# Optimization experiments

Hardware: AMD Instinct MI355X
Metric: run time of the kernel (lower is better)

## Reference

```python
import jax, jax.numpy as jnp
import numpy as np
import math

EMB = 2048
N_Q = 32
N_KV = 8
HEAD = EMB // N_Q  # 64
N_REP = N_Q // N_KV  # 4
B, T = 2, 2048
ROPE_BASE = 10000.0


def setup_inputs() -> dict:
    key = jax.random.key(0)
    ks = jax.random.split(key, 9)
    s = 0.02
    return {
        "x": jax.random.normal(ks[0], (B, T, EMB), jnp.float32),
        "Wq": jax.random.normal(ks[1], (EMB, EMB), jnp.float32) * s,
        "bq": jax.random.normal(ks[2], (EMB,), jnp.float32) * s,
        "Wk": jax.random.normal(ks[3], (EMB, N_KV * HEAD), jnp.float32) * s,
        "bk": jax.random.normal(ks[4], (N_KV * HEAD,), jnp.float32) * s,
        "Wv": jax.random.normal(ks[5], (EMB, N_KV * HEAD), jnp.float32) * s,
        "bv": jax.random.normal(ks[6], (N_KV * HEAD,), jnp.float32) * s,
        "Wo": jax.random.normal(ks[7], (EMB, EMB), jnp.float32) * s,
        "bo": jax.random.normal(ks[8], (EMB,), jnp.float32) * s,
    }


def _rope_cos_sin(t, dim, dtype):
    inv_freq = 1.0 / (ROPE_BASE ** (jnp.arange(0, dim, 2, dtype=jnp.float32) / dim))
    freqs = jnp.arange(t, dtype=jnp.float32)[:, None] * inv_freq[None, :]  # (T, D/2)
    emb = jnp.concatenate([freqs, freqs], axis=-1)  # (T, D)
    return jnp.cos(emb).astype(dtype), jnp.sin(emb).astype(dtype)


def _rotate_half(x):
    d = x.shape[-1] // 2
    return jnp.concatenate([-x[..., d:], x[..., :d]], axis=-1)


def reference(x, Wq, bq, Wk, bk, Wv, bv, Wo, bo):
    b, t, c = x.shape
    q = (x @ Wq + bq).reshape(b, t, N_Q, HEAD)
    k = (x @ Wk + bk).reshape(b, t, N_KV, HEAD)
    v = (x @ Wv + bv).reshape(b, t, N_KV, HEAD)

    cos, sin = _rope_cos_sin(t, HEAD, x.dtype)  # (T, HEAD)
    cos = cos[None, :, None, :]
    sin = sin[None, :, None, :]
    q = q * cos + _rotate_half(q) * sin
    k = k * cos + _rotate_half(k) * sin

    # (B, H, T, D)
    q = q.transpose(0, 2, 1, 3)
    k = k.transpose(0, 2, 1, 3)
    v = v.transpose(0, 2, 1, 3)

    # repeat_kv: expand kv heads to match query heads
    k = jnp.repeat(k, N_REP, axis=1)
    v = jnp.repeat(v, N_REP, axis=1)

    scale = 1.0 / math.sqrt(HEAD)
    att = jnp.einsum("bhqd,bhkd->bhqk", q, k) * scale
    causal = jnp.tril(jnp.ones((t, t), dtype=bool))
    att = jnp.where(causal[None, None], att, jnp.finfo(att.dtype).min)
    att = jax.nn.softmax(att, axis=-1)

    y = jnp.einsum("bhqk,bhkd->bhqd", att, v)
    y = y.transpose(0, 2, 1, 3).reshape(b, t, c)
    return y @ Wo + bo
```

## Files before the change

### kernel.cpp

```cpp
#include <hip/hip_runtime.h>
#include <hip/hip_bf16.h>
#include <cstdint>
#include <cstddef>

typedef __attribute__((ext_vector_type(4))) float f32x4;
typedef __attribute__((ext_vector_type(8))) short bf16x8;

#define B_    2
#define T_    2048
#define EMB_  2048
#define NQ_   32
#define NKV_  8
#define HEAD_ 64
#define NTOT_ 3072
#define M_    (B_ * T_)
#define QBLK_ 128
#define NK_   32

#define MFMA_ __builtin_amdgcn_mfma_f32_16x16x32_bf16

__device__ __forceinline__ unsigned short f2bf(float f) {
  union { float f; unsigned int u; } v; v.f = f;
  unsigned int r = v.u + 0x7fffu + ((v.u >> 16) & 1u);
  return (unsigned short)(r >> 16);
}

__device__ __forceinline__ float bf2f(unsigned short u) {
  union { unsigned int u; float f; } v; v.u = (unsigned int)u << 16; return v.f;
}

__device__ __forceinline__ unsigned int pk_bf16(float lo, float hi) {
  __hip_bfloat162 h = __float22bfloat162_rn(make_float2(lo, hi));
  union { __hip_bfloat162 h; unsigned int u; } c; c.h = h;
  return c.u;
}

__device__ __forceinline__ float ex2(float x) {
  float r;
  asm("v_exp_f32 %0, %1" : "=v"(r) : "v"(x));
  return r;
}

__device__ __forceinline__ void gload_lds16(const void* g, void* l) {
  __builtin_amdgcn_global_load_lds(
      (const __attribute__((address_space(1))) void*)g,
      (__attribute__((address_space(3))) void*)l, 16, 0, 0);
}


__global__ void cvt_bf16_kernel(const float* __restrict__ src,
                                unsigned short* __restrict__ dst, int n4) {
  int i = blockIdx.x * blockDim.x + threadIdx.x;
  if (i >= n4) return;
  float4 v = ((const float4*)src)[i];
  unsigned long long pk =
      (unsigned long long)f2bf(v.x) |
      ((unsigned long long)f2bf(v.y) << 16) |
      ((unsigned long long)f2bf(v.z) << 32) |
      ((unsigned long long)f2bf(v.w) << 48);
  *(unsigned long long*)(dst + (size_t)i * 4) = pk;
}

__global__ void transpose_cvt_kernel(const float* __restrict__ src,
                                     unsigned short* __restrict__ dst,
                                     int R, int C) {
  __shared__ float tile[32][33];
  int c0 = blockIdx.x * 32, r0 = blockIdx.y * 32;
  int tx = threadIdx.x, ty = threadIdx.y;
#pragma unroll
  for (int k = 0; k < 4; ++k)
    tile[ty + 8 * k][tx] = src[(size_t)(r0 + ty + 8 * k) * C + c0 + tx];
  __syncthreads();
#pragma unroll
  for (int k = 0; k < 4; ++k)
    dst[(size_t)(c0 + ty + 8 * k) * R + r0 + tx] = f2bf(tile[tx][ty + 8 * k]);
}

__global__ void concat_bias_kernel(const float* __restrict__ bq,
                                   const float* __restrict__ bk,
                                   const float* __restrict__ bv,
                                   float* __restrict__ dst) {
  int i = blockIdx.x * 256 + threadIdx.x;
  if (i < 2048) dst[i] = bq[i];
  else if (i < 2560) dst[i] = bk[i - 2048];
  else if (i < 3072) dst[i] = bv[i - 2560];
}

#define L2_10000 13.2877123795494f
#define QSCALE_  0.18033688011112043f

__global__ void rope_q_kernel(const unsigned short* __restrict__ qkv,
                              unsigned short* __restrict__ Qh) {
  int idx = blockIdx.x * 256 + threadIdx.x;
  int i  = idx & 31;
  int h  = (idx >> 5) & 31;
  int bt = idx >> 10;
  int t  = bt & (T_ - 1);
  int b  = bt >> 11;
  float invf = exp2f(-(float)i * (L2_10000 / 32.f));
  float ang = (float)t * invf;
  float s, c; sincosf(ang, &s, &c);
  const unsigned short* row = qkv + (size_t)bt * NTOT_ + h * 64;
  float x1 = bf2f(row[i]), x2 = bf2f(row[i + 32]);
  unsigned short* q = Qh + ((size_t)(b * NQ_ + h) * T_ + t) * HEAD_;
  q[i]      = f2bf((x1 * c - x2 * s) * QSCALE_);
  q[i + 32] = f2bf((x2 * c + x1 * s) * QSCALE_);
}

__global__ void rope_k_kernel(const unsigned short* __restrict__ qkv,
                              unsigned short* __restrict__ Kh) {
  int idx = blockIdx.x * 256 + threadIdx.x;
  int i  = idx & 31;
  int kh = (idx >> 5) & 7;
  int bt = idx >> 8;
  int t  = bt & (T_ - 1);
  int b  = bt >> 11;
  float invf = exp2f(-(float)i * (L2_10000 / 32.f));
  float ang = (float)t * invf;
  float s, c; sincosf(ang, &s, &c);
  const unsigned short* row = qkv + (size_t)bt * NTOT_ + 2048 + kh * 64;
  float x1 = bf2f(row[i]), x2 = bf2f(row[i + 32]);
  unsigned short* kp = Kh + ((size_t)(b * NKV_ + kh) * T_ + t) * HEAD_;
  kp[i]      = f2bf(x1 * c - x2 * s);
  kp[i + 32] = f2bf(x2 * c + x1 * s);
}

__global__ void vt_kernel(const unsigned short* __restrict__ qkv,
                          unsigned short* __restrict__ Vt) {
  int idx = blockIdx.x * 256 + threadIdx.x;
  int t  = idx & (T_ - 1);
  int d  = (idx >> 11) & 63;
  int kh = (idx >> 17) & 7;
  int b  = idx >> 20;
  Vt[((size_t)((b * NKV_ + kh) * 64 + d)) * T_ + t] =
      qkv[(size_t)(b * T_ + t) * NTOT_ + 2560 + kh * 64 + d];
}


__launch_bounds__(512, 4)
__global__ void gemm_qkv_3ph(const unsigned short* __restrict__ A,
                             const unsigned short* __restrict__ BT,
                             const float* __restrict__ bias,
                             unsigned short* __restrict__ C) {
  __shared__ unsigned short sh[2 * 20480];
  const int tid = threadIdx.x;
  const int lane = tid & 63, l16 = lane & 15, lg = lane >> 4;
  const int wave = tid >> 6, wm = wave >> 2, wn = wave & 3;
  const int bid = blockIdx.x;
  const int sw = (bid & 7) * 64 + (bid >> 3);
  const int mt = sw & 31, nt = sw >> 5;
  const int m0 = mt * 128, n0 = nt * 192;
  const int arow = tid >> 3;
  const int usrc = (tid & 7) ^ (arow & 7);
  const int swz = l16 & 7;
  const int uo0 = (lg ^ swz) << 3;
  const int uo1 = ((4 + lg) ^ swz) << 3;

  f32x4 acc[4][3];
#pragma unroll
  for (int i = 0; i < 4; ++i)
#pragma unroll
    for (int j = 0; j < 3; ++j) acc[i][j] = (f32x4){0.f, 0.f, 0.f, 0.f};

  auto STG = [&](int u) {
    if (u >= 5 * NK_) return;
    const int kt = u / 5, j = u % 5;
    char* bufb = (char*)sh + (kt & 1) * 40960;
    if (j < 2) {
      gload_lds16(A + (size_t)(m0 + j * 64 + arow) * 2048 + kt * 64 + usrc * 8,
                  bufb + j * 8192 + tid * 16);
    } else {
      const int jj = j - 2;
      gload_lds16(BT + (size_t)(n0 + jj * 64 + arow) * 2048 + kt * 64 + usrc * 8,
                  bufb + 16384 + jj * 8192 + tid * 16);
    }
  };

#pragma unroll
  for (int u = 0; u < 7; ++u) STG(u);
  asm volatile("s_waitcnt vmcnt(2)" ::: "memory");
  __builtin_amdgcn_s_barrier();

  for (int t = 0; t < NK_; ++t) {
    const unsigned short* Ab = sh + (t & 1) * 20480;
    const unsigned short* Bb = Ab + 8192;

    bf16x8 af[4][2], bfr[2];
#pragma unroll
    for (int fi = 0; fi < 4; ++fi) {
      const int ro = (fi * 32 + wm * 16 + l16) * 64;
      af[fi][0] = *(const bf16x8*)(Ab + ro + uo0);
      af[fi][1] = *(const bf16x8*)(Ab + ro + uo1);
    }
    {
      const int ro = (wn * 16 + l16) * 64;
      bfr[0] = *(const bf16x8*)(Bb + ro + uo0);
      bfr[1] = *(const bf16x8*)(Bb + ro + uo1);
    }
    STG(7 + 5 * t);  STG(8 + 5 * t);
    __builtin_amdgcn_s_barrier();
    asm volatile("s_waitcnt lgkmcnt(0)" ::: "memory");
    __builtin_amdgcn_sched_barrier(0);
    __builtin_amdgcn_s_setprio(1);
#pragma unroll
    for (int fi = 0; fi < 4; ++fi) {
      acc[fi][0] = MFMA_(af[fi][0], bfr[0], acc[fi][0], 0, 0, 0);
      acc[fi][0] = MFMA_(af[fi][1], bfr[1], acc[fi][0], 0, 0, 0);
    }
    __builtin_amdgcn_s_setprio(0);
    __builtin_amdgcn_s_barrier();

    {
      const int ro = (64 + wn * 16 + l16) * 64;
      bfr[0] = *(const bf16x8*)(Bb + ro + uo0);
      bfr[1] = *(const bf16x8*)(Bb + ro + uo1);
    }
    STG(9 + 5 * t);  STG(10 + 5 * t);
    __builtin_amdgcn_s_barrier();
    asm volatile("s_waitcnt lgkmcnt(0)" ::: "memory");
    __builtin_amdgcn_sched_barrier(0);
    __builtin_amdgcn_s_setprio(1);
#pragma unroll
    for (int fi = 0; fi < 4; ++fi) {
      acc[fi][1] = MFMA_(af[fi][0], bfr[0], acc[fi][1], 0, 0, 0);
      acc[fi][1] = MFMA_(af[fi][1], bfr[1], acc[fi][1], 0, 0, 0);
    }
    __builtin_amdgcn_s_setprio(0);
    __builtin_amdgcn_s_barrier();

    {
      const int ro = (128 + wn * 16 + l16) * 64;
      bfr[0] = *(const bf16x8*)(Bb + ro + uo0);
      bfr[1] = *(const bf16x8*)(Bb + ro + uo1);
    }
    STG(11 + 5 * t);
    __builtin_amdgcn_s_barrier();
    asm volatile("s_waitcnt lgkmcnt(0)" ::: "memory");
    __builtin_amdgcn_sched_barrier(0);
    __builtin_amdgcn_s_setprio(1);
#pragma unroll
    for (int fi = 0; fi < 4; ++fi) {
      acc[fi][2] = MFMA_(af[fi][0], bfr[0], acc[fi][2], 0, 0, 0);
      acc[fi][2] = MFMA_(af[fi][1], bfr[1], acc[fi][2], 0, 0, 0);
    }
    __builtin_amdgcn_s_setprio(0);
    if (t < NK_ - 2)       asm volatile("s_waitcnt vmcnt(2)" ::: "memory");
    else if (t == NK_ - 2) asm volatile("s_waitcnt vmcnt(0)" ::: "memory");
    __builtin_amdgcn_s_barrier();
  }

#pragma unroll
  for (int fj = 0; fj < 3; ++fj) {
    const int col = n0 + fj * 64 + wn * 16 + l16;
    const float bv = bias[col];
#pragma unroll
    for (int fi = 0; fi < 4; ++fi) {
      const int row0 = m0 + fi * 32 + wm * 16 + lg * 4;
#pragma unroll
      for (int r = 0; r < 4; ++r)
        C[(size_t)(row0 + r) * NTOT_ + col] = f2bf(acc[fi][fj][r] + bv);
    }
  }
}


__launch_bounds__(512, 2)
__global__ void gemm_o_2ph(const unsigned short* __restrict__ A,
                           const unsigned short* __restrict__ BT,
                           const float* __restrict__ bias,
                           float* __restrict__ C) {
  __shared__ unsigned short sh[2 * 24576];
  const int tid = threadIdx.x;
  const int lane = tid & 63, l16 = lane & 15, lg = lane >> 4;
  const int wave = tid >> 6, wm = wave >> 2, wn = wave & 3;
  const int bid = blockIdx.x;
  const int sw = (bid & 7) * 32 + (bid >> 3);
  const int mt = sw & 31, nt = sw >> 5;
  const int m0 = mt * 128, n0 = nt * 256;
  const int arow = tid >> 3;
  const int usrc = (tid & 7) ^ (arow & 7);
  const int swz = l16 & 7;
  const int uo0 = (lg ^ swz) << 3;
  const int uo1 = ((4 + lg) ^ swz) << 3;

  f32x4 acc[4][4];
#pragma unroll
  for (int i = 0; i < 4; ++i)
#pragma unroll
    for (int j = 0; j < 4; ++j) acc[i][j] = (f32x4){0.f, 0.f, 0.f, 0.f};

  auto STG = [&](int u) {
    if (u >= 6 * NK_) return;
    const int kt = u / 6, j = u % 6;
    char* bufb = (char*)sh + (kt & 1) * 49152;
    if (j < 2) {
      gload_lds16(A + (size_t)(m0 + j * 64 + arow) * 2048 + kt * 64 + usrc * 8,
                  bufb + j * 8192 + tid * 16);
    } else {
      const int jj = j - 2;
      gload_lds16(BT + (size_t)(n0 + jj * 64 + arow) * 2048 + kt * 64 + usrc * 8,
                  bufb + 16384 + jj * 8192 + tid * 16);
    }
  };

#pragma unroll
  for (int u = 0; u < 9; ++u) STG(u);
  asm volatile("s_waitcnt vmcnt(3)" ::: "memory");
  __builtin_amdgcn_s_barrier();

  for (int t = 0; t < NK_; ++t) {
    const unsigned short* Ab = sh + (t & 1) * 24576;
    const unsigned short* Bb = Ab + 8192;

    bf16x8 af[4][2], bfr[2][2];
#pragma unroll
    for (int fi = 0; fi < 4; ++fi) {
      const int ro = (fi * 32 + wm * 16 + l16) * 64;
      af[fi][0] = *(const bf16x8*)(Ab + ro + uo0);
      af[fi][1] = *(const bf16x8*)(Ab + ro + uo1);
    }
#pragma unroll
    for (int fj = 0; fj < 2; ++fj) {
      const int ro = (fj * 64 + wn * 16 + l16) * 64;
      bfr[fj][0] = *(const bf16x8*)(Bb + ro + uo0);
      bfr[fj][1] = *(const bf16x8*)(Bb + ro + uo1);
    }
    STG(9 + 6 * t);  STG(10 + 6 * t);  STG(11 + 6 * t);
    __builtin_amdgcn_s_barrier();
    asm volatile("s_waitcnt lgkmcnt(0)" ::: "memory");
    __builtin_amdgcn_sched_barrier(0);
    __builtin_amdgcn_s_setprio(1);
#pragma unroll
    for (int fi = 0; fi < 4; ++fi)
#pragma unroll
      for (int fj = 0; fj < 2; ++fj) {
        acc[fi][fj] = MFMA_(af[fi][0], bfr[fj][0], acc[fi][fj], 0, 0, 0);
        acc[fi][fj] = MFMA_(af[fi][1], bfr[fj][1], acc[fi][fj], 0, 0, 0);
      }
    __builtin_amdgcn_s_setprio(0);
    __builtin_amdgcn_s_barrier();

#pragma unroll
    for (int fj = 0; fj < 2; ++fj) {
      const int ro = ((2 + fj) * 64 + wn * 16 + l16) * 64;
      bfr[fj][0] = *(const bf16x8*)(Bb + ro + uo0);
      bfr[fj][1] = *(const bf16x8*)(Bb + ro + uo1);
    }
    STG(12 + 6 * t);  STG(13 + 6 * t);  STG(14 + 6 * t);
    __builtin_amdgcn_s_barrier();
    asm volatile("s_waitcnt lgkmcnt(0)" ::: "memory");
    __builtin_amdgcn_sched_barrier(0);
    __builtin_amdgcn_s_setprio(1);
#pragma unroll
    for (int fi = 0; fi < 4; ++fi)
#pragma unroll
      for (int fj = 0; fj < 2; ++fj) {
        acc[fi][2 + fj] = MFMA_(af[fi][0], bfr[fj][0], acc[fi][2 + fj], 0, 0, 0);
        acc[fi][2 + fj] = MFMA_(af[fi][1], bfr[fj][1], acc[fi][2 + fj], 0, 0, 0);
      }
    __builtin_amdgcn_s_setprio(0);
    if (t < NK_ - 2)       asm volatile("s_waitcnt vmcnt(3)" ::: "memory");
    else if (t == NK_ - 2) asm volatile("s_waitcnt vmcnt(0)" ::: "memory");
    __builtin_amdgcn_s_barrier();
  }

#pragma unroll
  for (int fj = 0; fj < 4; ++fj) {
    const int col = n0 + fj * 64 + wn * 16 + l16;
    const float bv = bias[col];
#pragma unroll
    for (int fi = 0; fi < 4; ++fi) {
      const int row0 = m0 + fi * 32 + wm * 16 + lg * 4;
#pragma unroll
      for (int r = 0; r < 4; ++r)
        C[(size_t)(row0 + r) * EMB_ + col] = acc[fi][fj][r] + bv;
    }
  }
}


__launch_bounds__(256, 2)
__global__ void flash_attn_kernel(const unsigned short* __restrict__ Qh,
                                  const unsigned short* __restrict__ Kh,
                                  const unsigned short* __restrict__ Vt,
                                  unsigned short* __restrict__ Y) {
  __shared__ unsigned short Klds[2][64 * 64];
  __shared__ unsigned short Vlds[2][64 * 64];
  __shared__ unsigned short Plds[4][32 * 64];
  const int tid = threadIdx.x;
  const int wave = tid >> 6, lane = tid & 63;
  const int l16 = lane & 15, lg = lane >> 4;
  const int h = blockIdx.y, b = blockIdx.z;
  const int kh = h >> 2;

  const size_t kbase = (size_t)(b * NKV_ + kh) * T_ * HEAD_;
  const size_t vbase = (size_t)(b * NKV_ + kh) * HEAD_ * T_;
  const int srow = tid >> 3;
  const int csrc = (tid & 7) ^ (srow & 7);
  unsigned short* pl = Plds[wave];
  const f32x4 zero4 = {0.f, 0.f, 0.f, 0.f};
  const short one_bf = (short)0x3F80;
  const bf16x8 onesv = {one_bf, one_bf, one_bf, one_bf,
                        one_bf, one_bf, one_bf, one_bf};

#define STAGE(bi, kv0) do {                                                         \
    gload_lds16(Kh + kbase + (size_t)((kv0) + srow) * HEAD_ + csrc * 8,             \
                (char*)Klds[bi] + tid * 16);                                        \
    gload_lds16(Kh + kbase + (size_t)((kv0) + srow + 32) * HEAD_ + csrc * 8,        \
                (char*)Klds[bi] + 4096 + tid * 16);                                 \
    gload_lds16(Vt + vbase + (size_t)srow * T_ + (kv0) + csrc * 8,                  \
                (char*)Vlds[bi] + tid * 16);                                        \
    gload_lds16(Vt + vbase + (size_t)(srow + 32) * T_ + (kv0) + csrc * 8,           \
                (char*)Vlds[bi] + 4096 + tid * 16);                                 \
  } while (0)

  for (int seg = 0; seg < 2; ++seg) {
    const int qt = seg ? (15 - (int)blockIdx.x) : (int)blockIdx.x;
    const int q0 = qt * QBLK_;
    const int nt = (q0 >> 6) + 2;

    bf16x8 aq[2][2];
#pragma unroll
    for (int qh = 0; qh < 2; ++qh) {
      const unsigned short* qp =
          Qh + ((size_t)(b * NQ_ + h) * T_ + q0 + wave * 32 + qh * 16 + l16) * HEAD_;
      aq[qh][0] = *(const bf16x8*)(qp + lg * 8);
      aq[qh][1] = *(const bf16x8*)(qp + 32 + lg * 8);
    }

    f32x4 oacc[2][4];
    f32x4 lsum[2];
#pragma unroll
    for (int qh = 0; qh < 2; ++qh) {
      lsum[qh] = zero4;
#pragma unroll
      for (int df = 0; df < 4; ++df) oacc[qh][df] = zero4;
    }
    float mreg[2] = {-1e30f, -1e30f};

    STAGE(0, 0);

    for (int t = 0; t < nt; ++t) {
      if (t + 1 < nt) {
        STAGE((t + 1) & 1, (t + 1) * 64);
        asm volatile("s_waitcnt vmcnt(4)" ::: "memory");
      } else {
        asm volatile("s_waitcnt vmcnt(0)" ::: "memory");
      }
      __builtin_amdgcn_s_barrier();
      __builtin_amdgcn_sched_barrier(0);

      const unsigned short* Kb = Klds[t & 1];
      const unsigned short* Vb = Vlds[t & 1];
      const int kv0 = t * 64;

      float p[2][4][4];
#pragma unroll
      for (int cf = 0; cf < 4; ++cf) {
        const int krow = cf * 16 + l16;
        const bf16x8 k0 = *(const bf16x8*)(Kb + krow * 64 + ((lg ^ (krow & 7)) << 3));
        const bf16x8 k1 = *(const bf16x8*)(Kb + krow * 64 + (((4 + lg) ^ (krow & 7)) << 3));
#pragma unroll
        for (int qh = 0; qh < 2; ++qh) {
          f32x4 z = zero4;
          z = MFMA_(k0, aq[qh][0], z, 0, 0, 0);
          z = MFMA_(k1, aq[qh][1], z, 0, 0, 0);
#pragma unroll
          for (int r = 0; r < 4; ++r) p[qh][cf][r] = z[r];
        }
      }

      if (t >= nt - 2) {
#pragma unroll
        for (int qh = 0; qh < 2; ++qh) {
          const int qg = q0 + wave * 32 + qh * 16 + l16;
#pragma unroll
          for (int cf = 0; cf < 4; ++cf)
#pragma unroll
            for (int r = 0; r < 4; ++r)
              if (kv0 + cf * 16 + lg * 4 + r > qg) p[qh][cf][r] = -1e30f;
        }
      }

      float mn[2];
#pragma unroll
      for (int qh = 0; qh < 2; ++qh) {
        float m = mreg[qh];
#pragma unroll
        for (int cf = 0; cf < 4; ++cf) {
          m = fmaxf(m, fmaxf(p[qh][cf][0], p[qh][cf][1]));
          m = fmaxf(m, fmaxf(p[qh][cf][2], p[qh][cf][3]));
        }
        m = fmaxf(m, __shfl_xor(m, 16, 64));
        m = fmaxf(m, __shfl_xor(m, 32, 64));
        mn[qh] = m;
      }

      const float dmax = fmaxf(mn[0] - mreg[0], mn[1] - mreg[1]);
      if (!__all(dmax <= 8.f)) {
#pragma unroll
        for (int qh = 0; qh < 2; ++qh) {
          const float corr = ex2(mreg[qh] - mn[qh]);
          mreg[qh] = mn[qh];
          lsum[qh][0] *= corr;
#pragma unroll
          for (int df = 0; df < 4; ++df)
#pragma unroll
            for (int r = 0; r < 4; ++r) oacc[qh][df][r] *= corr;
        }
      }

#pragma unroll
      for (int qh = 0; qh < 2; ++qh)
#pragma unroll
        for (int cf = 0; cf < 4; ++cf)
#pragma unroll
          for (int r = 0; r < 4; ++r)
            p[qh][cf][r] = ex2(p[qh][cf][r] - mreg[qh]);

#pragma unroll
      for (int qh = 0; qh < 2; ++qh) {
        const int row = qh * 16 + l16;
#pragma unroll
        for (int cf = 0; cf < 4; ++cf) {
          const unsigned int w0 = pk_bf16(p[qh][cf][0], p[qh][cf][1]);
          const unsigned int w1 = pk_bf16(p[qh][cf][2], p[qh][cf][3]);
          const int u = cf * 2 + (lg >> 1);
          char* ad = (char*)pl + row * 128 + ((u ^ (row & 7)) << 4) + ((lg & 1) << 3);
          *(unsigned long long*)ad =
              (unsigned long long)w0 | ((unsigned long long)w1 << 32);
        }
      }
      bf16x8 pf[2][2];
#pragma unroll
      for (int qh = 0; qh < 2; ++qh) {
        const int row = qh * 16 + l16;
#pragma unroll
        for (int k2 = 0; k2 < 2; ++k2) {
          const int u = k2 * 4 + lg;
          pf[qh][k2] = *(const bf16x8*)((char*)pl + row * 128 + ((u ^ (row & 7)) << 4));
        }
      }

#pragma unroll
      for (int qh = 0; qh < 2; ++qh) {
        lsum[qh] = MFMA_(onesv, pf[qh][0], lsum[qh], 0, 0, 0);
        lsum[qh] = MFMA_(onesv, pf[qh][1], lsum[qh], 0, 0, 0);
      }
#pragma unroll
      for (int df = 0; df < 4; ++df) {
        const int vrow = df * 16 + l16;
        const bf16x8 v0 = *(const bf16x8*)(Vb + vrow * 64 + ((lg ^ (vrow & 7)) << 3));
        const bf16x8 v1 = *(const bf16x8*)(Vb + vrow * 64 + (((4 + lg) ^ (vrow & 7)) << 3));
#pragma unroll
        for (int qh = 0; qh < 2; ++qh) {
          oacc[qh][df] = MFMA_(v0, pf[qh][0], oacc[qh][df], 0, 0, 0);
          oacc[qh][df] = MFMA_(v1, pf[qh][1], oacc[qh][df], 0, 0, 0);
        }
      }

      asm volatile("s_waitcnt lgkmcnt(0)" ::: "memory");
      __builtin_amdgcn_sched_barrier(0);
      __builtin_amdgcn_s_barrier();
    }

#pragma unroll
    for (int qh = 0; qh < 2; ++qh) {
      const float inv = 1.f / lsum[qh][0];
      const int tq = q0 + wave * 32 + qh * 16 + l16;
      unsigned short* yp = Y + ((size_t)(b * T_ + tq)) * EMB_ + h * HEAD_;
#pragma unroll
      for (int df = 0; df < 4; ++df) {
        const unsigned int w0 = pk_bf16(oacc[qh][df][0] * inv, oacc[qh][df][1] * inv);
        const unsigned int w1 = pk_bf16(oacc[qh][df][2] * inv, oacc[qh][df][3] * inv);
        *(unsigned long long*)(yp + df * 16 + lg * 4) =
            (unsigned long long)w0 | ((unsigned long long)w1 << 32);
      }
    }
  }
#undef STAGE
}


extern "C" void kernel_launch(void* const* d_in, const int* in_sizes, int n_in,
                              void* d_out, int out_size, void* d_ws, size_t ws_size,
                              hipStream_t stream) {
  const float* x  = (const float*)d_in[0];
  const float* Wq = (const float*)d_in[1];
  const float* bq = (const float*)d_in[2];
  const float* Wk = (const float*)d_in[3];
  const float* bk = (const float*)d_in[4];
  const float* Wv = (const float*)d_in[5];
  const float* bv = (const float*)d_in[6];
  const float* Wo = (const float*)d_in[7];
  const float* bo = (const float*)d_in[8];
  float* out = (float*)d_out;

  char* ws = (char*)d_ws;
  size_t off = 0;
  auto alloc = [&](size_t bytes) {
    void* p = ws + off;
    off += (bytes + 255) & ~(size_t)255;
    return p;
  };
  unsigned short* xb     = (unsigned short*)alloc((size_t)M_ * EMB_ * 2);
  unsigned short* WqkvT  = (unsigned short*)alloc((size_t)NTOT_ * EMB_ * 2);
  unsigned short* WoT    = (unsigned short*)alloc((size_t)EMB_ * EMB_ * 2);
  float*          bcat   = (float*)alloc((size_t)NTOT_ * 4);
  unsigned short* QKVlin = (unsigned short*)alloc((size_t)M_ * NTOT_ * 2);
  unsigned short* Qh     = (unsigned short*)alloc((size_t)B_ * NQ_ * T_ * HEAD_ * 2);
  unsigned short* Kh     = (unsigned short*)alloc((size_t)B_ * NKV_ * T_ * HEAD_ * 2);
  unsigned short* Vt     = (unsigned short*)alloc((size_t)B_ * NKV_ * HEAD_ * T_ * 2);
  unsigned short* Yb     = (unsigned short*)alloc((size_t)M_ * EMB_ * 2);

  cvt_bf16_kernel<<<(M_ * EMB_ / 4 + 255) / 256, 256, 0, stream>>>(x, xb, M_ * EMB_ / 4);

  dim3 tb(32, 8);
  transpose_cvt_kernel<<<dim3(EMB_ / 32, EMB_ / 32), tb, 0, stream>>>(Wq, WqkvT, EMB_, EMB_);
  transpose_cvt_kernel<<<dim3(512 / 32, EMB_ / 32), tb, 0, stream>>>(Wk, WqkvT + (size_t)2048 * 2048, EMB_, 512);
  transpose_cvt_kernel<<<dim3(512 / 32, EMB_ / 32), tb, 0, stream>>>(Wv, WqkvT + (size_t)2560 * 2048, EMB_, 512);
  transpose_cvt_kernel<<<dim3(EMB_ / 32, EMB_ / 32), tb, 0, stream>>>(Wo, WoT, EMB_, EMB_);
  concat_bias_kernel<<<(NTOT_ + 255) / 256, 256, 0, stream>>>(bq, bk, bv, bcat);

  gemm_qkv_3ph<<<512, 512, 0, stream>>>(xb, WqkvT, bcat, QKVlin);

  rope_q_kernel<<<(B_ * T_ * NQ_ * 32) / 256, 256, 0, stream>>>(QKVlin, Qh);
  rope_k_kernel<<<(B_ * T_ * NKV_ * 32) / 256, 256, 0, stream>>>(QKVlin, Kh);
  vt_kernel<<<(B_ * NKV_ * HEAD_ * T_) / 256, 256, 0, stream>>>(QKVlin, Vt);

  flash_attn_kernel<<<dim3(8, NQ_, B_), 256, 0, stream>>>(Qh, Kh, Vt, Yb);

  gemm_o_2ph<<<256, 512, 0, stream>>>(Yb, WoT, bo, out);

  (void)in_sizes; (void)n_in; (void)out_size; (void)ws_size;
}
```

Baseline: 223.8 us.

## Shrink flash-attention query block to 64 rows, one 16-row tile per wave

Halves the query block per workgroup from 128 to 64 rows, so each wave handles a single 16-row query tile instead of two. The grid doubles along the query axis and the per-block causal tile count becomes qt+1, with masking needed only on the last KV tile. This raises parallelism and cuts registers and LDS per block, which can improve occupancy and load balance. The cost is that each K/V tile staged in LDS is reused by half as many queries, which doubles K/V global and LDS traffic.

```diff
diff --git a/kernel.cpp b/kernel.cpp
--- a/kernel.cpp
+++ b/kernel.cpp
@@ -14,7 +14,7 @@
 #define HEAD_ 64
 #define NTOT_ 3072
 #define M_    (B_ * T_)
-#define QBLK_ 128
+#define QBLK_ 64
 #define NK_   32
 
 #define MFMA_ __builtin_amdgcn_mfma_f32_16x16x32_bf16
@@ -386,7 +386,7 @@
                                   unsigned short* __restrict__ Y) {
   __shared__ unsigned short Klds[2][64 * 64];
   __shared__ unsigned short Vlds[2][64 * 64];
-  __shared__ unsigned short Plds[4][32 * 64];
+  __shared__ unsigned short Plds[4][16 * 64];
   const int tid = threadIdx.x;
   const int wave = tid >> 6, lane = tid & 63;
   const int l16 = lane & 15, lg = lane >> 4;
@@ -415,28 +415,23 @@
   } while (0)
 
   for (int seg = 0; seg < 2; ++seg) {
-    const int qt = seg ? (15 - (int)blockIdx.x) : (int)blockIdx.x;
+    const int qt = seg ? (31 - (int)blockIdx.x) : (int)blockIdx.x;
     const int q0 = qt * QBLK_;
-    const int nt = (q0 >> 6) + 2;
-
-    bf16x8 aq[2][2];
-#pragma unroll
-    for (int qh = 0; qh < 2; ++qh) {
+    const int nt = qt + 1;
+
+    bf16x8 aq0, aq1;
+    {
       const unsigned short* qp =
-          Qh + ((size_t)(b * NQ_ + h) * T_ + q0 + wave * 32 + qh * 16 + l16) * HEAD_;
-      aq[qh][0] = *(const bf16x8*)(qp + lg * 8);
-      aq[qh][1] = *(const bf16x8*)(qp + 32 + lg * 8);
-    }
-
-    f32x4 oacc[2][4];
-    f32x4 lsum[2];
-#pragma unroll
-    for (int qh = 0; qh < 2; ++qh) {
-      lsum[qh] = zero4;
-#pragma unroll
-      for (int df = 0; df < 4; ++df) oacc[qh][df] = zero4;
-    }
-    float mreg[2] = {-1e30f, -1e30f};
+          Qh + ((size_t)(b * NQ_ + h) * T_ + q0 + wave * 16 + l16) * HEAD_;
+      aq0 = *(const bf16x8*)(qp + lg * 8);
+      aq1 = *(const bf16x8*)(qp + 32 + lg * 8);
+    }
+
+    f32x4 oacc[4];
+    f32x4 lsum = zero4;
+#pragma unroll
+    for (int df = 0; df < 4; ++df) oacc[df] = zero4;
+    float mreg = -1e30f;
 
     STAGE(0, 0);
 
@@ -454,109 +449,79 @@
       const unsigned short* Vb = Vlds[t & 1];
       const int kv0 = t * 64;
 
-      float p[2][4][4];
+      float p[4][4];
 #pragma unroll
       for (int cf = 0; cf < 4; ++cf) {
         const int krow = cf * 16 + l16;
         const bf16x8 k0 = *(const bf16x8*)(Kb + krow * 64 + ((lg ^ (krow & 7)) << 3));
         const bf16x8 k1 = *(const bf16x8*)(Kb + krow * 64 + (((4 + lg) ^ (krow & 7)) << 3));
-#pragma unroll
-        for (int qh = 0; qh < 2; ++qh) {
-          f32x4 z = zero4;
-          z = MFMA_(k0, aq[qh][0], z, 0, 0, 0);
-          z = MFMA_(k1, aq[qh][1], z, 0, 0, 0);
-#pragma unroll
-          for (int r = 0; r < 4; ++r) p[qh][cf][r] = z[r];
-        }
-      }
-
-      if (t >= nt - 2) {
-#pragma unroll
-        for (int qh = 0; qh < 2; ++qh) {
-          const int qg = q0 + wave * 32 + qh * 16 + l16;
-#pragma unroll
-          for (int cf = 0; cf < 4; ++cf)
-#pragma unroll
-            for (int r = 0; r < 4; ++r)
-              if (kv0 + cf * 16 + lg * 4 + r > qg) p[qh][cf][r] = -1e30f;
-        }
-      }
-
-      float mn[2];
-#pragma unroll
-      for (int qh = 0; qh < 2; ++qh) {
-        float m = mreg[qh];
-#pragma unroll
-        for (int cf = 0; cf < 4; ++cf) {
-          m = fmaxf(m, fmaxf(p[qh][cf][0], p[qh][cf][1]));
-          m = fmaxf(m, fmaxf(p[qh][cf][2], p[qh][cf][3]));
-        }
-        m = fmaxf(m, __shfl_xor(m, 16, 64));
-        m = fmaxf(m, __shfl_xor(m, 32, 64));
-        mn[qh] = m;
-      }
-
-      const float dmax = fmaxf(mn[0] - mreg[0], mn[1] - mreg[1]);
-      if (!__all(dmax <= 8.f)) {
-#pragma unroll
-        for (int qh = 0; qh < 2; ++qh) {
-          const float corr = ex2(mreg[qh] - mn[qh]);
-          mreg[qh] = mn[qh];
-          lsum[qh][0] *= corr;
-#pragma unroll
-          for (int df = 0; df < 4; ++df)
-#pragma unroll
-            for (int r = 0; r < 4; ++r) oacc[qh][df][r] *= corr;
-        }
-      }
-
-#pragma unroll
-      for (int qh = 0; qh < 2; ++qh)
+        f32x4 z = zero4;
+        z = MFMA_(k0, aq0, z, 0, 0, 0);
+        z = MFMA_(k1, aq1, z, 0, 0, 0);
+#pragma unroll
+        for (int r = 0; r < 4; ++r) p[cf][r] = z[r];
+      }
+
+      if (t == nt - 1) {
+        const int qg = q0 + wave * 16 + l16;
 #pragma unroll
         for (int cf = 0; cf < 4; ++cf)
 #pragma unroll
           for (int r = 0; r < 4; ++r)
-            p[qh][cf][r] = ex2(p[qh][cf][r] - mreg[qh]);
-
-#pragma unroll
-      for (int qh = 0; qh < 2; ++qh) {
-        const int row = qh * 16 + l16;
-#pragma unroll
-        for (int cf = 0; cf < 4; ++cf) {
-          const unsigned int w0 = pk_bf16(p[qh][cf][0], p[qh][cf][1]);
-          const unsigned int w1 = pk_bf16(p[qh][cf][2], p[qh][cf][3]);
-          const int u = cf * 2 + (lg >> 1);
-          char* ad = (char*)pl + row * 128 + ((u ^ (row & 7)) << 4) + ((lg & 1) << 3);
-          *(unsigned long long*)ad =
-              (unsigned long long)w0 | ((unsigned long long)w1 << 32);
-        }
-      }
-      bf16x8 pf[2][2];
-#pragma unroll
-      for (int qh = 0; qh < 2; ++qh) {
-        const int row = qh * 16 + l16;
-#pragma unroll
-        for (int k2 = 0; k2 < 2; ++k2) {
-          const int u = k2 * 4 + lg;
-          pf[qh][k2] = *(const bf16x8*)((char*)pl + row * 128 + ((u ^ (row & 7)) << 4));
-        }
-      }
-
-#pragma unroll
-      for (int qh = 0; qh < 2; ++qh) {
-        lsum[qh] = MFMA_(onesv, pf[qh][0], lsum[qh], 0, 0, 0);
-        lsum[qh] = MFMA_(onesv, pf[qh][1], lsum[qh], 0, 0, 0);
-      }
+            if (kv0 + cf * 16 + lg * 4 + r > qg) p[cf][r] = -1e30f;
+      }
+
+      float m = mreg;
+#pragma unroll
+      for (int cf = 0; cf < 4; ++cf) {
+        m = fmaxf(m, fmaxf(p[cf][0], p[cf][1]));
+        m = fmaxf(m, fmaxf(p[cf][2], p[cf][3]));
+      }
+      m = fmaxf(m, __shfl_xor(m, 16, 64));
+      m = fmaxf(m, __shfl_xor(m, 32, 64));
+
+      if (!__all(m - mreg <= 8.f)) {
+        const float corr = ex2(mreg - m);
+        mreg = m;
+        lsum[0] *= corr;
+#pragma unroll
+        for (int df = 0; df < 4; ++df)
+#pragma unroll
+          for (int r = 0; r < 4; ++r) oacc[df][r] *= corr;
+      }
+
+#pragma unroll
+      for (int cf = 0; cf < 4; ++cf)
+#pragma unroll
+        for (int r = 0; r < 4; ++r)
+          p[cf][r] = ex2(p[cf][r] - mreg);
+
+      const int row = l16;
+#pragma unroll
+      for (int cf = 0; cf < 4; ++cf) {
+        const unsigned int w0 = pk_bf16(p[cf][0], p[cf][1]);
+        const unsigned int w1 = pk_bf16(p[cf][2], p[cf][3]);
+        const int u = cf * 2 + (lg >> 1);
+        char* ad = (char*)pl + row * 128 + ((u ^ (row & 7)) << 4) + ((lg & 1) << 3);
+        *(unsigned long long*)ad =
+            (unsigned long long)w0 | ((unsigned long long)w1 << 32);
+      }
+      bf16x8 pf[2];
+#pragma unroll
+      for (int k2 = 0; k2 < 2; ++k2) {
+        const int u = k2 * 4 + lg;
+        pf[k2] = *(const bf16x8*)((char*)pl + row * 128 + ((u ^ (row & 7)) << 4));
+      }
+
+      lsum = MFMA_(onesv, pf[0], lsum, 0, 0, 0);
+      lsum = MFMA_(onesv, pf[1], lsum, 0, 0, 0);
 #pragma unroll
       for (int df = 0; df < 4; ++df) {
         const int vrow = df * 16 + l16;
         const bf16x8 v0 = *(const bf16x8*)(Vb + vrow * 64 + ((lg ^ (vrow & 7)) << 3));
         const bf16x8 v1 = *(const bf16x8*)(Vb + vrow * 64 + (((4 + lg) ^ (vrow & 7)) << 3));
-#pragma unroll
-        for (int qh = 0; qh < 2; ++qh) {
-          oacc[qh][df] = MFMA_(v0, pf[qh][0], oacc[qh][df], 0, 0, 0);
-          oacc[qh][df] = MFMA_(v1, pf[qh][1], oacc[qh][df], 0, 0, 0);
-        }
+        oacc[df] = MFMA_(v0, pf[0], oacc[df], 0, 0, 0);
+        oacc[df] = MFMA_(v1, pf[1], oacc[df], 0, 0, 0);
       }
 
       asm volatile("s_waitcnt lgkmcnt(0)" ::: "memory");
@@ -564,15 +529,14 @@
       __builtin_amdgcn_s_barrier();
     }
 
-#pragma unroll
-    for (int qh = 0; qh < 2; ++qh) {
-      const float inv = 1.f / lsum[qh][0];
-      const int tq = q0 + wave * 32 + qh * 16 + l16;
+    {
+      const float inv = 1.f / lsum[0];
+      const int tq = q0 + wave * 16 + l16;
       unsigned short* yp = Y + ((size_t)(b * T_ + tq)) * EMB_ + h * HEAD_;
 #pragma unroll
       for (int df = 0; df < 4; ++df) {
-        const unsigned int w0 = pk_bf16(oacc[qh][df][0] * inv, oacc[qh][df][1] * inv);
-        const unsigned int w1 = pk_bf16(oacc[qh][df][2] * inv, oacc[qh][df][3] * inv);
+        const unsigned int w0 = pk_bf16(oacc[df][0] * inv, oacc[df][1] * inv);
+        const unsigned int w1 = pk_bf16(oacc[df][2] * inv, oacc[df][3] * inv);
         *(unsigned long long*)(yp + df * 16 + lg * 4) =
             (unsigned long long)w0 | ((unsigned long long)w1 << 32);
       }
@@ -628,7 +592,7 @@
   rope_k_kernel<<<(B_ * T_ * NKV_ * 32) / 256, 256, 0, stream>>>(QKVlin, Kh);
   vt_kernel<<<(B_ * NKV_ * HEAD_ * T_) / 256, 256, 0, stream>>>(QKVlin, Vt);
 
-  flash_attn_kernel<<<dim3(8, NQ_, B_), 256, 0, stream>>>(Qh, Kh, Vt, Yb);
+  flash_attn_kernel<<<dim3(16, NQ_, B_), 256, 0, stream>>>(Qh, Kh, Vt, Yb);
 
   gemm_o_2ph<<<256, 512, 0, stream>>>(Yb, WoT, bo, out);
 
```

Measured after the change: 220.2 us. Within noise of the previous version (-1.6%).
